# Kernel optimization log

Measured on AMD Instinct MI355X. Metric: run time of the kernel, lower is better.

Reference implementation:

```python
import jax, jax.numpy as jnp
import numpy as np

B, S, IN_DIM, D_MODEL, H = 8, 1024, 512, 1024, 16
DEPTH = D_MODEL // H
LN_EPS = 1e-5


def setup_inputs() -> dict:
    key = jax.random.key(0)
    ks = jax.random.split(key, 10)
    def xavier(k, shape):
        fan_in, fan_out = shape[0], shape[1]
        lim = float(np.sqrt(6.0 / (fan_in + fan_out)))
        return jax.random.uniform(k, shape, jnp.float32, -lim, lim)
    return {
        "x": jax.random.normal(ks[0], (B, S, IN_DIM), jnp.float32),
        "mask": jax.random.randint(ks[1], (H, S, S), 0, 2, jnp.int32),
        "wq_w": xavier(ks[2], (IN_DIM, D_MODEL)),
        "wq_b": jnp.zeros((D_MODEL,), jnp.float32),
        "wk_w": xavier(ks[3], (IN_DIM, D_MODEL)),
        "wk_b": jnp.zeros((D_MODEL,), jnp.float32),
        "wv_w": xavier(ks[4], (IN_DIM, D_MODEL)),
        "wv_b": jnp.zeros((D_MODEL,), jnp.float32),
        "dense_w": xavier(ks[5], (D_MODEL, D_MODEL)),
        "dense_b": jnp.zeros((D_MODEL,), jnp.float32),
        "res_w": xavier(ks[6], (IN_DIM, D_MODEL)),  # residual_linear (no bias)
        "ln_g": 1.0 + 0.02 * jax.random.normal(ks[7], (D_MODEL,), jnp.float32),
        "ln_b": 0.02 * jax.random.normal(ks[8], (D_MODEL,), jnp.float32),
    }


def reference(x, mask, wq_w, wq_b, wk_w, wk_b, wv_w, wv_b,
              dense_w, dense_b, res_w, ln_g, ln_b):
    bs = x.shape[0]
    residual = x @ res_w  # [B,S,D_MODEL]
    # project and split heads -> [B,H,S,depth]
    def split(t):
        return t.reshape(bs, -1, H, DEPTH).transpose(0, 2, 1, 3)
    q = split(x @ wq_w + wq_b)
    k = split(x @ wk_w + wk_b)
    v = split(x @ wv_w + wv_b)
    scale = 1.0 / jnp.sqrt(jnp.asarray(DEPTH, x.dtype))
    attn = jnp.einsum("bhqd,bhkd->bhqk", q, k) * scale
    attn = jnp.where(mask[None] == 0, jnp.asarray(-1e9, attn.dtype), attn)
    attn = jax.nn.softmax(attn, axis=-1)  # dropout is identity in eval
    out = jnp.einsum("bhqk,bhkd->bhqd", attn, v)
    out = out.transpose(0, 2, 1, 3).reshape(bs, -1, D_MODEL)
    out = out @ dense_w + dense_b
    # residual + LayerNorm
    y = residual + out
    mu = jnp.mean(y, axis=-1, keepdims=True)
    var = jnp.mean(jnp.square(y - mu), axis=-1, keepdims=True)
    y = (y - mu) * jax.lax.rsqrt(var + LN_EPS)
    return y * ln_g + ln_b
```

## Files before the change

kernel.cpp:

```cpp
#include <hip/hip_runtime.h>
#include <stdint.h>

#define B_ 8
#define S_ 1024
#define IN_DIM 512
#define DM 1024
#define H_ 16
#define DEP 64

typedef __bf16 bf16;
typedef __attribute__((ext_vector_type(8))) __bf16 bf16x8;
typedef __attribute__((ext_vector_type(4))) __bf16 bf16x4;
typedef __attribute__((ext_vector_type(4))) short short4v;
typedef __attribute__((ext_vector_type(4))) float f32x4;

#if defined(__has_builtin)
#if __has_builtin(__builtin_amdgcn_mfma_f32_16x16x16_bf16)
#define HAVE_NEW16 1
#endif
#endif
static __device__ __forceinline__ f32x4 mfma16(bf16x4 a, bf16x4 b, f32x4 c) {
#ifdef HAVE_NEW16
    return __builtin_amdgcn_mfma_f32_16x16x16_bf16(a, b, c, 0, 0, 0);
#else
    union { bf16x4 h; short4v s; } ua, ub;
    ua.h = a; ub.h = b;
    return __builtin_amdgcn_mfma_f32_16x16x16bf16_1k(ua.s, ub.s, c, 0, 0, 0);
#endif
}

static __device__ __forceinline__ void gld_lds16(const void* g, void* l) {
    __builtin_amdgcn_global_load_lds(
        (const __attribute__((address_space(1))) uint32_t*)g,
        (__attribute__((address_space(3))) uint32_t*)l, 16, 0, 0);
}

__global__ void detect_kernel(const uint16_t* __restrict__ xraw, int* __restrict__ flag) {
    const int t = threadIdx.x;
    int sane = 0;
    #pragma unroll
    for (int j = 0; j < 8; j++) {
        const uint16_t u = xraw[t * 8 + j];
        const int e = (u >> 7) & 0xff;
        sane += ((u & 0x7fff) == 0 || (e >= 100 && e <= 140)) ? 1 : 0;
    }
    #pragma unroll
    for (int m = 1; m < 64; m <<= 1) sane += __shfl_xor(sane, m);
    if (t == 0) *flag = (sane >= 450) ? 1 : 0;
}

static __device__ __forceinline__ float ldin(const void* p, size_t i, int isb) {
    return isb ? (float)((const bf16*)p)[i] : ((const float*)p)[i];
}

__global__ __launch_bounds__(256) void transpose_kernel(
    const void* __restrict__ wq, const void* __restrict__ wk, const void* __restrict__ wv,
    const void* __restrict__ res, const void* __restrict__ dense,
    bf16* __restrict__ wqT, bf16* __restrict__ wkT, bf16* __restrict__ wvT,
    bf16* __restrict__ resT, bf16* __restrict__ denseT, const int* __restrict__ flag)
{
    const int isb = *flag;
    __shared__ bf16 tile[32][33];
    const int z = blockIdx.z;
    const void* src; bf16* dst; int kb, kd;
    if (z == 0)      { src = wq;    dst = wqT;    kb = 0;   kd = 512;  }
    else if (z == 1) { src = wk;    dst = wkT;    kb = 0;   kd = 512;  }
    else if (z == 2) { src = wv;    dst = wvT;    kb = 0;   kd = 512;  }
    else if (z == 3) { src = res;   dst = resT;   kb = 0;   kd = 512;  }
    else if (z == 4) { src = dense; dst = denseT; kb = 0;   kd = 1024; }
    else             { src = dense; dst = denseT; kb = 512; kd = 1024; }
    const int n0 = blockIdx.x * 32, k0 = blockIdx.y * 32;
    const int tx = threadIdx.x, ty = threadIdx.y;
    #pragma unroll
    for (int r = 0; r < 4; r++)
        tile[ty + r*8][tx] = (bf16)ldin(src, (size_t)(kb + k0 + ty + r*8) * DM + n0 + tx, isb);
    __syncthreads();
    #pragma unroll
    for (int r = 0; r < 4; r++)
        dst[(size_t)(n0 + ty + r*8) * kd + kb + k0 + tx] = tile[tx][ty + r*8];
}

__global__ __launch_bounds__(256) void xconv_kernel(
    const void* __restrict__ x, bf16* __restrict__ xc, const int* __restrict__ flag)
{
    const int isb = *flag;
    const size_t i = ((size_t)blockIdx.x * 256 + threadIdx.x) * 4;
    #pragma unroll
    for (int j = 0; j < 4; j++) xc[i + j] = (bf16)ldin(x, i + j, isb);
}

__global__ __launch_bounds__(256) void smallconv_kernel(
    const void* b0, const void* b1, const void* b2, const void* b3,
    const void* b4, const void* b5, bf16* __restrict__ out, const int* __restrict__ flag)
{
    const int isb = *flag;
    const void* srcs[6] = {b0, b1, b2, b3, b4, b5};
    const void* s = srcs[blockIdx.x];
    for (int i = threadIdx.x; i < 1024; i += 256)
        out[blockIdx.x * 1024 + i] = (bf16)ldin(s, i, isb);
}

__global__ __launch_bounds__(256) void maskpack_kernel(
    const int* __restrict__ mask, unsigned long long* __restrict__ mb)
{
    const int w = threadIdx.x >> 6, lane = threadIdx.x & 63;
    const int gw = blockIdx.x * 4 + w;
    for (int c = gw; c < 262144; c += 4096) {
        const int v = mask[(size_t)c * 64 + lane];
        const unsigned long long bits = __ballot(v != 0);
        if (lane == 0) mb[c] = bits;
    }
}

template<int KDIM>
static __device__ __forceinline__ void gemm_core(
    const bf16* __restrict__ A, const bf16* __restrict__ BT,
    int m0, int n0, bf16* Asm, bf16* Bsm, f32x4 acc[4][4])
{
    const int tid = threadIdx.x, l = tid & 63, w = tid >> 6;
    const int wm = w >> 1, wn = w & 1, quad = l >> 4, l15 = l & 15;
    #pragma unroll
    for (int i = 0; i < 4; i++)
        #pragma unroll
        for (int j = 0; j < 4; j++) acc[i][j] = f32x4{0.f, 0.f, 0.f, 0.f};

    for (int k0 = 0; k0 < KDIM; k0 += 32) {
        __syncthreads();
        #pragma unroll
        for (int qq = 0; qq < 2; qq++) {
            const int c = qq*256 + tid;
            const int row = c >> 2, ch = c & 3;
            gld_lds16(A  + (size_t)(m0 + row)*KDIM + k0 + ch*8, Asm + (qq*256 + w*64)*8);
            gld_lds16(BT + (size_t)(n0 + row)*KDIM + k0 + ch*8, Bsm + (qq*256 + w*64)*8);
        }
        __syncthreads();
        bf16x8 af[4], bfv[4];
        #pragma unroll
        for (int i = 0; i < 4; i++)
            af[i] = *(const bf16x8*)(Asm + (wm*64 + i*16 + l15)*32 + quad*8);
        #pragma unroll
        for (int j = 0; j < 4; j++)
            bfv[j] = *(const bf16x8*)(Bsm + (wn*64 + j*16 + l15)*32 + quad*8);
        #pragma unroll
        for (int i = 0; i < 4; i++)
            #pragma unroll
            for (int j = 0; j < 4; j++)
                acc[i][j] = __builtin_amdgcn_mfma_f32_16x16x32_bf16(af[i], bfv[j], acc[i][j], 0, 0, 0);
    }
}

#define EPI_P 132
__global__ __launch_bounds__(256) void proj_kernel(
    const bf16* __restrict__ x,
    const bf16* __restrict__ wqT, const bf16* __restrict__ wkT,
    const bf16* __restrict__ wvT, const bf16* __restrict__ resT,
    const bf16* __restrict__ small,
    bf16* __restrict__ Q, bf16* __restrict__ K, bf16* __restrict__ VtG, bf16* __restrict__ R)
{
    __shared__ alignas(16) char smem[17408];
    bf16* Asm = (bf16*)smem;
    bf16* Bsm = (bf16*)(smem + 8192);
    bf16* epi = (bf16*)smem;

    const int m0 = blockIdx.x * 128;
    const int ng = blockIdx.y * 128;
    const int sel = ng >> 10, n0 = ng & 1023;
    const bf16* BT; const bf16* bias = nullptr;
    if (sel == 0)      { BT = wqT; bias = small;        }
    else if (sel == 1) { BT = wkT; bias = small + 1024; }
    else if (sel == 2) { BT = wvT; bias = small + 2048; }
    else               { BT = resT; }

    f32x4 acc[4][4];
    gemm_core<IN_DIM>(x, BT, m0, n0, Asm, Bsm, acc);

    const int tid = threadIdx.x, l = tid & 63, w = tid >> 6;
    const int wm = w >> 1, wn = w & 1, quad = l >> 4, l15 = l & 15;

    if (sel == 2) {
        const int bb = m0 >> 10, srow0 = m0 & 1023;
        #pragma unroll
        for (int hf = 0; hf < 2; hf++) {
            __syncthreads();
            if (wn == hf) {
                #pragma unroll
                for (int j = 0; j < 4; j++) {
                    const int cl = j*16 + l15;
                    const float bv = (float)bias[n0 + hf*64 + cl];
                    #pragma unroll
                    for (int i = 0; i < 4; i++) {
                        const int rho = wm*64 + i*16 + quad*4;
                        #pragma unroll
                        for (int r = 0; r < 4; r++)
                            epi[cl*EPI_P + rho + r] = (bf16)(acc[i][j][r] + bv);
                    }
                }
            }
            __syncthreads();
            const int hh = (n0 >> 6) + hf;
            const int sc = tid & 15;
            #pragma unroll
            for (int pass = 0; pass < 4; pass++) {
                const int dl = (tid >> 4) + pass*16;
                bf16x8 v;
                #pragma unroll
                for (int k = 0; k < 8; k++) v[k] = epi[dl*EPI_P + sc*8 + k];
                *(bf16x8*)(VtG + ((size_t)(bb*16 + hh)*64 + dl)*S_ + srow0 + sc*8) = v;
            }
        }
        return;
    }

    #pragma unroll
    for (int j = 0; j < 4; j++) {
        const int col = n0 + wn*64 + j*16 + l15;
        const float bv = (sel < 3) ? (float)bias[col] : 0.f;
        #pragma unroll
        for (int i = 0; i < 4; i++) {
            const int rb = m0 + wm*64 + i*16 + quad*4;
            #pragma unroll
            for (int r = 0; r < 4; r++) {
                const float v = acc[i][j][r] + bv;
                if (sel == 0)      Q[(size_t)(rb + r)*DM + col] = (bf16)(v * 0.125f);
                else if (sel == 1) K[(size_t)(rb + r)*DM + col] = (bf16)v;
                else               R[(size_t)(rb + r)*DM + col] = (bf16)v;
            }
        }
    }
}

#define KP 68
__global__ __launch_bounds__(256) void attn_kernel(
    const bf16* __restrict__ Q, const bf16* __restrict__ K, const bf16* __restrict__ VtG,
    const unsigned long long* __restrict__ mb, bf16* __restrict__ AO)
{
    __shared__ alignas(16) bf16 Ksm[64*KP];
    __shared__ alignas(16) bf16 Vsm[64*KP];

    const int tid = threadIdx.x, l = tid & 63, w = tid >> 6;
    const int quad = l >> 4, l15 = l & 15;
    const int b = blockIdx.y >> 4, h = blockIdx.y & 15;
    const int wrow = blockIdx.x*128 + w*32;
    const size_t rowbase = (size_t)b * S_;

    bf16x8 qa[2][2];
    #pragma unroll
    for (int g = 0; g < 2; g++) {
        const bf16* qp = Q + (rowbase + wrow + g*16 + l15)*DM + h*DEP + quad*8;
        qa[g][0] = *(const bf16x8*)qp;
        qa[g][1] = *(const bf16x8*)(qp + 32);
    }
    const bf16* kgbase = K + rowbase*DM + h*DEP;
    const bf16* vgbase = VtG + (size_t)(b*16 + h)*64*S_;
    const unsigned long long* mbase[2];
    #pragma unroll
    for (int g = 0; g < 2; g++)
        mbase[g] = mb + ((size_t)h*S_ + wrow + g*16 + l15) * 16;

    f32x4 oT[2][4];
    float lsum[2] = {0.f, 0.f};
    #pragma unroll
    for (int g = 0; g < 2; g++)
        #pragma unroll
        for (int dt = 0; dt < 4; dt++) oT[g][dt] = f32x4{0.f,0.f,0.f,0.f};

    const int srow = tid >> 3, sch = tid & 7;

    bf16x8 k0v = *(const bf16x8*)(kgbase + (size_t)srow*DM + sch*8);
    bf16x8 k1v = *(const bf16x8*)(kgbase + (size_t)(32 + srow)*DM + sch*8);
    bf16x8 v0v = *(const bf16x8*)(vgbase + (size_t)srow*S_ + sch*8);
    bf16x8 v1v = *(const bf16x8*)(vgbase + (size_t)(32 + srow)*S_ + sch*8);
    uint32_t mlo[2], mhi[2];
    #pragma unroll
    for (int g = 0; g < 2; g++) {
        const unsigned long long mword = mbase[g][0];
        mlo[g] = (uint32_t)mword; mhi[g] = (uint32_t)(mword >> 32);
    }

    for (int it = 0; it < 16; it++) {
        __syncthreads();
        *(bf16x8*)(Ksm + srow*KP + sch*8)        = k0v;
        *(bf16x8*)(Ksm + (32 + srow)*KP + sch*8) = k1v;
        *(bf16x8*)(Vsm + srow*KP + sch*8)        = v0v;
        *(bf16x8*)(Vsm + (32 + srow)*KP + sch*8) = v1v;
        __syncthreads();

        const uint32_t cmlo[2] = {mlo[0], mlo[1]}, cmhi[2] = {mhi[0], mhi[1]};
        if (it + 1 < 16) {
            const int nkt = (it + 1) * 64;
            k0v = *(const bf16x8*)(kgbase + (size_t)(nkt + srow)*DM + sch*8);
            k1v = *(const bf16x8*)(kgbase + (size_t)(nkt + 32 + srow)*DM + sch*8);
            v0v = *(const bf16x8*)(vgbase + (size_t)srow*S_ + nkt + sch*8);
            v1v = *(const bf16x8*)(vgbase + (size_t)(32 + srow)*S_ + nkt + sch*8);
            #pragma unroll
            for (int g = 0; g < 2; g++) {
                const unsigned long long mword = mbase[g][it + 1];
                mlo[g] = (uint32_t)mword; mhi[g] = (uint32_t)(mword >> 32);
            }
        }

        #pragma unroll
        for (int sub = 0; sub < 2; sub++) {
            bf16x8 kf[2][2];
            bf16x4 va[2][4];
            #pragma unroll
            for (int h2 = 0; h2 < 2; h2++) {
                const bf16* kp = Ksm + (sub*32 + h2*16 + l15)*KP + quad*8;
                kf[h2][0] = *(const bf16x8*)kp;
                kf[h2][1] = *(const bf16x8*)(kp + 32);
            }
            #pragma unroll
            for (int h2 = 0; h2 < 2; h2++)
                #pragma unroll
                for (int dt = 0; dt < 4; dt++)
                    va[h2][dt] = *(const bf16x4*)(Vsm + (dt*16 + l15)*KP + sub*32 + h2*16 + quad*4);

            #pragma unroll
            for (int g = 0; g < 2; g++) {
                f32x4 st[2];
                #pragma unroll
                for (int h2 = 0; h2 < 2; h2++) {
                    f32x4 z = {0.f,0.f,0.f,0.f};
                    z = __builtin_amdgcn_mfma_f32_16x16x32_bf16(kf[h2][0], qa[g][0], z, 0, 0, 0);
                    z = __builtin_amdgcn_mfma_f32_16x16x32_bf16(kf[h2][1], qa[g][1], z, 0, 0, 0);
                    st[h2] = z;
                }
                const uint32_t msk = sub ? cmhi[g] : cmlo[g];
                bf16x4 pb[2];
                #pragma unroll
                for (int h2 = 0; h2 < 2; h2++) {
                    const uint32_t nib = (msk >> (h2*16 + quad*4)) & 0xfu;
                    #pragma unroll
                    for (int r = 0; r < 4; r++) {
                        const float e = __expf(st[h2][r]);
                        const float pv = ((nib >> r) & 1u) ? e : 0.f;
                        lsum[g] += pv;
                        pb[h2][r] = (bf16)pv;
                    }
                }
                #pragma unroll
                for (int h2 = 0; h2 < 2; h2++)
                    #pragma unroll
                    for (int dt = 0; dt < 4; dt++)
                        oT[g][dt] = mfma16(va[h2][dt], pb[h2], oT[g][dt]);
            }
        }
    }

    #pragma unroll
    for (int g = 0; g < 2; g++) {
        lsum[g] += __shfl_xor(lsum[g], 16);
        lsum[g] += __shfl_xor(lsum[g], 32);
        const float inv = 1.0f / lsum[g];
        bf16* aor = AO + (rowbase + wrow + g*16 + l15)*DM + h*DEP;
        #pragma unroll
        for (int dt = 0; dt < 4; dt++) {
            bf16x4 ov;
            #pragma unroll
            for (int r = 0; r < 4; r++) ov[r] = (bf16)(oT[g][dt][r] * inv);
            *(bf16x4*)(aor + dt*16 + quad*4) = ov;
        }
    }
}

__global__ __launch_bounds__(256) void dense_kernel(
    const bf16* __restrict__ AOin, const bf16* __restrict__ dT,
    const bf16* __restrict__ db, bf16* __restrict__ R)
{
    __shared__ alignas(16) bf16 Asm[128*32];
    __shared__ alignas(16) bf16 Bsm[128*32];
    const int m0 = blockIdx.x * 128, n0 = blockIdx.y * 128;
    f32x4 acc[4][4];
    gemm_core<DM>(AOin, dT, m0, n0, Asm, Bsm, acc);
    const int tid = threadIdx.x, l = tid & 63, w = tid >> 6;
    const int wm = w >> 1, wn = w & 1, quad = l >> 4, l15 = l & 15;
    #pragma unroll
    for (int j = 0; j < 4; j++) {
        const int col = n0 + wn*64 + j*16 + l15;
        const float bv = (float)db[col];
        #pragma unroll
        for (int i = 0; i < 4; i++) {
            const int rb = m0 + wm*64 + i*16 + quad*4;
            #pragma unroll
            for (int r = 0; r < 4; r++) {
                const size_t idx = (size_t)(rb + r)*DM + col;
                R[idx] = (bf16)((float)R[idx] + acc[i][j][r] + bv);
            }
        }
    }
}

__global__ __launch_bounds__(256) void ln_kernel(
    const bf16* __restrict__ R, const bf16* __restrict__ small,
    void* __restrict__ out, const int* __restrict__ flag)
{
    const int isb = *flag;
    __shared__ float red[8];
    const int row = blockIdx.x, tid = threadIdx.x;
    const bf16x4 rv = *(const bf16x4*)(R + (size_t)row*DM + tid*4);
    const float vx = (float)rv[0], vy = (float)rv[1], vz = (float)rv[2], vw = (float)rv[3];
    float s = vx + vy + vz + vw;
    #pragma unroll
    for (int m = 1; m < 64; m <<= 1) s += __shfl_xor(s, m);
    const int w = tid >> 6;
    if ((tid & 63) == 0) red[w] = s;
    __syncthreads();
    const float mu = (red[0] + red[1] + red[2] + red[3]) * (1.0f/DM);
    const float dx = vx - mu, dy = vy - mu, dz = vz - mu, dw = vw - mu;
    float q = dx*dx + dy*dy + dz*dz + dw*dw;
    #pragma unroll
    for (int m = 1; m < 64; m <<= 1) q += __shfl_xor(q, m);
    if ((tid & 63) == 0) red[4 + w] = q;
    __syncthreads();
    const float var = (red[4] + red[5] + red[6] + red[7]) * (1.0f/DM);
    const float rstd = rsqrtf(var + 1e-5f);
    const int col = tid * 4;
    const bf16x4 gv = *(const bf16x4*)(small + 4*1024 + col);
    const bf16x4 bv = *(const bf16x4*)(small + 5*1024 + col);
    const float o0 = dx*rstd*(float)gv[0] + (float)bv[0];
    const float o1 = dy*rstd*(float)gv[1] + (float)bv[1];
    const float o2 = dz*rstd*(float)gv[2] + (float)bv[2];
    const float o3 = dw*rstd*(float)gv[3] + (float)bv[3];
    if (isb) {
        bf16x4 ov; ov[0] = (bf16)o0; ov[1] = (bf16)o1; ov[2] = (bf16)o2; ov[3] = (bf16)o3;
        *(bf16x4*)((bf16*)out + (size_t)row*DM + col) = ov;
    } else {
        float4 ov = {o0, o1, o2, o3};
        *(float4*)((float*)out + (size_t)row*DM + col) = ov;
    }
}

extern "C" void kernel_launch(void* const* d_in, const int* in_sizes, int n_in,
                              void* d_out, int out_size, void* d_ws, size_t ws_size,
                              hipStream_t stream) {
    const int* mask = (const int*)d_in[1];

    char* ws = (char*)d_ws;
    bf16* wqT   = (bf16*)(ws);
    bf16* wkT   = (bf16*)(ws + ((size_t)1 << 20));
    bf16* wvT   = (bf16*)(ws + ((size_t)2 << 20));
    bf16* resT  = (bf16*)(ws + ((size_t)3 << 20));
    bf16* dT    = (bf16*)(ws + ((size_t)4 << 20));
    bf16* small = (bf16*)(ws + ((size_t)6 << 20));
    int*  flag  = (int*) (ws + ((size_t)6 << 20) + 16384);
    unsigned long long* mbits = (unsigned long long*)(ws + ((size_t)7 << 20));
    bf16* Qb    = (bf16*)(ws + ((size_t)9  << 20));
    bf16* Kb    = (bf16*)(ws + ((size_t)25 << 20));
    bf16* VtG   = (bf16*)(ws + ((size_t)41 << 20));
    bf16* R     = (bf16*)(ws + ((size_t)57 << 20));
    bf16* xc    = (bf16*)d_out;

    detect_kernel<<<1, 64, 0, stream>>>((const uint16_t*)d_in[0], flag);
    transpose_kernel<<<dim3(32, 16, 6), dim3(32, 8), 0, stream>>>(
        d_in[2], d_in[4], d_in[6], d_in[10], d_in[8],
        wqT, wkT, wvT, resT, dT, flag);
    xconv_kernel<<<4096, 256, 0, stream>>>(d_in[0], xc, flag);
    smallconv_kernel<<<6, 256, 0, stream>>>(
        d_in[3], d_in[5], d_in[7], d_in[9], d_in[11], d_in[12], small, flag);
    maskpack_kernel<<<1024, 256, 0, stream>>>(mask, mbits);
    proj_kernel<<<dim3(64, 32), 256, 0, stream>>>(
        xc, wqT, wkT, wvT, resT, small, Qb, Kb, VtG, R);
    attn_kernel<<<dim3(8, 128), 256, 0, stream>>>(Qb, Kb, VtG, mbits, Qb );
    dense_kernel<<<dim3(64, 8), 256, 0, stream>>>(Qb, dT, small + 3*1024, R);
    ln_kernel<<<8192, 256, 0, stream>>>(R, small, d_out, flag);
}
```

Measured before the change: 372.2 us.

## Fuse prep kernels, drop LDS staging in attention, use exp2 with prescaled Q

Merges the detect, transpose, x-convert, bias-convert and mask-pack launches into one prep kernel, with every block redoing the dtype detection locally. Attention now loads K and V fragments straight from global memory into registers, double-buffered across 32-key sub-steps, instead of staging them in shared memory behind barriers. Softmax uses the hardware exp2 with log2(e) folded into the Q scale. The trade-off is more uncoalesced global reads per wave, relying on cache reuse, plus redundant detection work in every prep and LayerNorm block.

```diff
diff --git a/kernel.cpp b/kernel.cpp
--- a/kernel.cpp
+++ b/kernel.cpp
@@ -29,86 +29,96 @@
 #endif
 }
 
+static __device__ __forceinline__ float fexp2(float x) {
+#if defined(__has_builtin)
+#if __has_builtin(__builtin_amdgcn_exp2f)
+    return __builtin_amdgcn_exp2f(x);
+#define FEXP_DONE 1
+#endif
+#endif
+#ifndef FEXP_DONE
+    float r; __asm__("v_exp_f32 %0, %1" : "=v"(r) : "v"(x)); return r;
+#endif
+}
+
 static __device__ __forceinline__ void gld_lds16(const void* g, void* l) {
     __builtin_amdgcn_global_load_lds(
         (const __attribute__((address_space(1))) uint32_t*)g,
         (__attribute__((address_space(3))) uint32_t*)l, 16, 0, 0);
 }
 
-__global__ void detect_kernel(const uint16_t* __restrict__ xraw, int* __restrict__ flag) {
-    const int t = threadIdx.x;
+static __device__ __forceinline__ float ldin(const void* p, size_t i, int isb) {
+    return isb ? (float)((const bf16*)p)[i] : ((const float*)p)[i];
+}
+
+static __device__ __forceinline__ int block_detect(const void* x, int tid, int* sred) {
+    const uint32_t two = ((const uint32_t*)x)[tid];
     int sane = 0;
     #pragma unroll
-    for (int j = 0; j < 8; j++) {
-        const uint16_t u = xraw[t * 8 + j];
+    for (int half = 0; half < 2; half++) {
+        const uint32_t u = (half ? (two >> 16) : two) & 0xffffu;
         const int e = (u >> 7) & 0xff;
         sane += ((u & 0x7fff) == 0 || (e >= 100 && e <= 140)) ? 1 : 0;
     }
     #pragma unroll
-    for (int m = 1; m < 64; m <<= 1) sane += __shfl_xor(sane, m);
-    if (t == 0) *flag = (sane >= 450) ? 1 : 0;
-}
-
-static __device__ __forceinline__ float ldin(const void* p, size_t i, int isb) {
-    return isb ? (float)((const bf16*)p)[i] : ((const float*)p)[i];
-}
-
-__global__ __launch_bounds__(256) void transpose_kernel(
+    for (int m2 = 1; m2 < 64; m2 <<= 1) sane += __shfl_xor(sane, m2);
+    if ((tid & 63) == 0) sred[tid >> 6] = sane;
+    __syncthreads();
+    return (sred[0] + sred[1] + sred[2] + sred[3]) >= 900;
+}
+
+__global__ __launch_bounds__(256) void prep_kernel(
+    const void* __restrict__ x, const int* __restrict__ mask,
     const void* __restrict__ wq, const void* __restrict__ wk, const void* __restrict__ wv,
     const void* __restrict__ res, const void* __restrict__ dense,
+    const void* __restrict__ bq, const void* __restrict__ bk, const void* __restrict__ bv,
+    const void* __restrict__ bd, const void* __restrict__ lg, const void* __restrict__ lb,
     bf16* __restrict__ wqT, bf16* __restrict__ wkT, bf16* __restrict__ wvT,
-    bf16* __restrict__ resT, bf16* __restrict__ denseT, const int* __restrict__ flag)
-{
-    const int isb = *flag;
+    bf16* __restrict__ resT, bf16* __restrict__ denseT,
+    bf16* __restrict__ xc, bf16* __restrict__ small, unsigned long long* __restrict__ mb)
+{
     __shared__ bf16 tile[32][33];
-    const int z = blockIdx.z;
-    const void* src; bf16* dst; int kb, kd;
-    if (z == 0)      { src = wq;    dst = wqT;    kb = 0;   kd = 512;  }
-    else if (z == 1) { src = wk;    dst = wkT;    kb = 0;   kd = 512;  }
-    else if (z == 2) { src = wv;    dst = wvT;    kb = 0;   kd = 512;  }
-    else if (z == 3) { src = res;   dst = resT;   kb = 0;   kd = 512;  }
-    else if (z == 4) { src = dense; dst = denseT; kb = 0;   kd = 1024; }
-    else             { src = dense; dst = denseT; kb = 512; kd = 1024; }
-    const int n0 = blockIdx.x * 32, k0 = blockIdx.y * 32;
-    const int tx = threadIdx.x, ty = threadIdx.y;
-    #pragma unroll
-    for (int r = 0; r < 4; r++)
-        tile[ty + r*8][tx] = (bf16)ldin(src, (size_t)(kb + k0 + ty + r*8) * DM + n0 + tx, isb);
-    __syncthreads();
-    #pragma unroll
-    for (int r = 0; r < 4; r++)
-        dst[(size_t)(n0 + ty + r*8) * kd + kb + k0 + tx] = tile[tx][ty + r*8];
-}
-
-__global__ __launch_bounds__(256) void xconv_kernel(
-    const void* __restrict__ x, bf16* __restrict__ xc, const int* __restrict__ flag)
-{
-    const int isb = *flag;
-    const size_t i = ((size_t)blockIdx.x * 256 + threadIdx.x) * 4;
-    #pragma unroll
-    for (int j = 0; j < 4; j++) xc[i + j] = (bf16)ldin(x, i + j, isb);
-}
-
-__global__ __launch_bounds__(256) void smallconv_kernel(
-    const void* b0, const void* b1, const void* b2, const void* b3,
-    const void* b4, const void* b5, bf16* __restrict__ out, const int* __restrict__ flag)
-{
-    const int isb = *flag;
-    const void* srcs[6] = {b0, b1, b2, b3, b4, b5};
-    const void* s = srcs[blockIdx.x];
-    for (int i = threadIdx.x; i < 1024; i += 256)
-        out[blockIdx.x * 1024 + i] = (bf16)ldin(s, i, isb);
-}
-
-__global__ __launch_bounds__(256) void maskpack_kernel(
-    const int* __restrict__ mask, unsigned long long* __restrict__ mb)
-{
-    const int w = threadIdx.x >> 6, lane = threadIdx.x & 63;
-    const int gw = blockIdx.x * 4 + w;
-    for (int c = gw; c < 262144; c += 4096) {
-        const int v = mask[(size_t)c * 64 + lane];
-        const unsigned long long bits = __ballot(v != 0);
-        if (lane == 0) mb[c] = bits;
+    __shared__ int sred[4];
+    const int tid = threadIdx.x;
+    const int isb = block_detect(x, tid, sred);
+    const int idx = blockIdx.x;
+
+    if (idx < 3072) {
+        const int z = idx >> 9, r2 = idx & 511;
+        const void* src; bf16* dst; int kb, kd;
+        if (z == 0)      { src = wq;    dst = wqT;    kb = 0;   kd = 512;  }
+        else if (z == 1) { src = wk;    dst = wkT;    kb = 0;   kd = 512;  }
+        else if (z == 2) { src = wv;    dst = wvT;    kb = 0;   kd = 512;  }
+        else if (z == 3) { src = res;   dst = resT;   kb = 0;   kd = 512;  }
+        else if (z == 4) { src = dense; dst = denseT; kb = 0;   kd = 1024; }
+        else             { src = dense; dst = denseT; kb = 512; kd = 1024; }
+        const int n0 = (r2 & 31) * 32, k0 = (r2 >> 5) * 32;
+        const int tx = tid & 31, ty = tid >> 5;
+        #pragma unroll
+        for (int r = 0; r < 4; r++)
+            tile[ty + r*8][tx] = (bf16)ldin(src, (size_t)(kb + k0 + ty + r*8) * DM + n0 + tx, isb);
+        __syncthreads();
+        #pragma unroll
+        for (int r = 0; r < 4; r++)
+            dst[(size_t)(n0 + ty + r*8) * kd + kb + k0 + tx] = tile[tx][ty + r*8];
+    } else if (idx < 7168) {
+        const size_t i = ((size_t)(idx - 3072) * 256 + tid) * 4;
+        #pragma unroll
+        for (int j = 0; j < 4; j++) xc[i + j] = (bf16)ldin(x, i + j, isb);
+    } else if (idx < 8192) {
+        const int w = tid >> 6, lane = tid & 63;
+        const int gw = (idx - 7168) * 4 + w;
+        for (int c = gw; c < 262144; c += 4096) {
+            const int v = mask[(size_t)c * 64 + lane];
+            const unsigned long long bits = __ballot(v != 0);
+            if (lane == 0) mb[c] = bits;
+        }
+    } else {
+        const void* srcs[6] = {bq, bk, bv, bd, lg, lb};
+        const int s = idx - 8192;
+        const void* sp = srcs[s];
+        for (int i = tid; i < 1024; i += 256)
+            small[s * 1024 + i] = (bf16)ldin(sp, i, isb);
     }
 }
 
@@ -221,7 +231,7 @@
             #pragma unroll
             for (int r = 0; r < 4; r++) {
                 const float v = acc[i][j][r] + bv;
-                if (sel == 0)      Q[(size_t)(rb + r)*DM + col] = (bf16)(v * 0.125f);
+                if (sel == 0)      Q[(size_t)(rb + r)*DM + col] = (bf16)(v * 0.180336881f);
                 else if (sel == 1) K[(size_t)(rb + r)*DM + col] = (bf16)v;
                 else               R[(size_t)(rb + r)*DM + col] = (bf16)v;
             }
@@ -229,14 +239,51 @@
     }
 }
 
-#define KP 68
+#define ATTN_PRE(KF, VA)                                                        \
+  do {                                                                          \
+    KF[0][0] = *(const bf16x8*)(kb0);  KF[0][1] = *(const bf16x8*)(kb0 + 32);   \
+    KF[1][0] = *(const bf16x8*)(kb1);  KF[1][1] = *(const bf16x8*)(kb1 + 32);   \
+    _Pragma("unroll")                                                           \
+    for (int dt = 0; dt < 4; dt++) {                                            \
+      VA[0][dt] = *(const bf16x4*)(vb[dt]);                                     \
+      VA[1][dt] = *(const bf16x4*)(vb[dt] + 16);                                \
+    }                                                                           \
+    kb0 += 32*DM; kb1 += 32*DM;                                                 \
+    _Pragma("unroll")                                                           \
+    for (int dt = 0; dt < 4; dt++) vb[dt] += 32;                                \
+  } while (0)
+
+#define ATTN_STEP(KF, VA, M0, M1)                                               \
+  do {                                                                          \
+    _Pragma("unroll")                                                           \
+    for (int g = 0; g < 2; g++) {                                               \
+      f32x4 st0 = {0.f,0.f,0.f,0.f}, st1 = {0.f,0.f,0.f,0.f};                   \
+      st0 = __builtin_amdgcn_mfma_f32_16x16x32_bf16(KF[0][0], qa[g][0], st0, 0,0,0); \
+      st0 = __builtin_amdgcn_mfma_f32_16x16x32_bf16(KF[0][1], qa[g][1], st0, 0,0,0); \
+      st1 = __builtin_amdgcn_mfma_f32_16x16x32_bf16(KF[1][0], qa[g][0], st1, 0,0,0); \
+      st1 = __builtin_amdgcn_mfma_f32_16x16x32_bf16(KF[1][1], qa[g][1], st1, 0,0,0); \
+      const uint32_t msk_ = g ? (M1) : (M0);                                    \
+      const uint32_t nib0 = (msk_ >> (quad*4)) & 0xfu;                          \
+      const uint32_t nib1 = (msk_ >> (16 + quad*4)) & 0xfu;                     \
+      bf16x4 pb0, pb1;                                                          \
+      _Pragma("unroll")                                                         \
+      for (int r = 0; r < 4; r++) {                                             \
+        float e0 = fexp2(st0[r]); e0 = ((nib0 >> r) & 1u) ? e0 : 0.f;           \
+        float e1 = fexp2(st1[r]); e1 = ((nib1 >> r) & 1u) ? e1 : 0.f;           \
+        lsum[g] += e0 + e1; pb0[r] = (bf16)e0; pb1[r] = (bf16)e1;               \
+      }                                                                         \
+      _Pragma("unroll")                                                         \
+      for (int dt = 0; dt < 4; dt++) {                                          \
+        oT[g][dt] = mfma16(VA[0][dt], pb0, oT[g][dt]);                          \
+        oT[g][dt] = mfma16(VA[1][dt], pb1, oT[g][dt]);                          \
+      }                                                                         \
+    }                                                                           \
+  } while (0)
+
 __global__ __launch_bounds__(256) void attn_kernel(
     const bf16* __restrict__ Q, const bf16* __restrict__ K, const bf16* __restrict__ VtG,
     const unsigned long long* __restrict__ mb, bf16* __restrict__ AO)
 {
-    __shared__ alignas(16) bf16 Ksm[64*KP];
-    __shared__ alignas(16) bf16 Vsm[64*KP];
-
     const int tid = threadIdx.x, l = tid & 63, w = tid >> 6;
     const int quad = l >> 4, l15 = l & 15;
     const int b = blockIdx.y >> 4, h = blockIdx.y & 15;
@@ -250,8 +297,13 @@
         qa[g][0] = *(const bf16x8*)qp;
         qa[g][1] = *(const bf16x8*)(qp + 32);
     }
-    const bf16* kgbase = K + rowbase*DM + h*DEP;
-    const bf16* vgbase = VtG + (size_t)(b*16 + h)*64*S_;
+    const bf16* kb0 = K + (rowbase + l15)*DM + h*DEP + quad*8;
+    const bf16* kb1 = kb0 + 16*DM;
+    const bf16* vb[4];
+    #pragma unroll
+    for (int dt = 0; dt < 4; dt++)
+        vb[dt] = VtG + ((size_t)(b*16 + h)*64 + dt*16 + l15)*S_ + quad*4;
+
     const unsigned long long* mbase[2];
     #pragma unroll
     for (int g = 0; g < 2; g++)
@@ -264,87 +316,23 @@
         #pragma unroll
         for (int dt = 0; dt < 4; dt++) oT[g][dt] = f32x4{0.f,0.f,0.f,0.f};
 
-    const int srow = tid >> 3, sch = tid & 7;
-
-    bf16x8 k0v = *(const bf16x8*)(kgbase + (size_t)srow*DM + sch*8);
-    bf16x8 k1v = *(const bf16x8*)(kgbase + (size_t)(32 + srow)*DM + sch*8);
-    bf16x8 v0v = *(const bf16x8*)(vgbase + (size_t)srow*S_ + sch*8);
-    bf16x8 v1v = *(const bf16x8*)(vgbase + (size_t)(32 + srow)*S_ + sch*8);
-    uint32_t mlo[2], mhi[2];
-    #pragma unroll
-    for (int g = 0; g < 2; g++) {
-        const unsigned long long mword = mbase[g][0];
-        mlo[g] = (uint32_t)mword; mhi[g] = (uint32_t)(mword >> 32);
-    }
-
-    for (int it = 0; it < 16; it++) {
-        __syncthreads();
-        *(bf16x8*)(Ksm + srow*KP + sch*8)        = k0v;
-        *(bf16x8*)(Ksm + (32 + srow)*KP + sch*8) = k1v;
-        *(bf16x8*)(Vsm + srow*KP + sch*8)        = v0v;
-        *(bf16x8*)(Vsm + (32 + srow)*KP + sch*8) = v1v;
-        __syncthreads();
-
-        const uint32_t cmlo[2] = {mlo[0], mlo[1]}, cmhi[2] = {mhi[0], mhi[1]};
-        if (it + 1 < 16) {
-            const int nkt = (it + 1) * 64;
-            k0v = *(const bf16x8*)(kgbase + (size_t)(nkt + srow)*DM + sch*8);
-            k1v = *(const bf16x8*)(kgbase + (size_t)(nkt + 32 + srow)*DM + sch*8);
-            v0v = *(const bf16x8*)(vgbase + (size_t)srow*S_ + nkt + sch*8);
-            v1v = *(const bf16x8*)(vgbase + (size_t)(32 + srow)*S_ + nkt + sch*8);
-            #pragma unroll
-            for (int g = 0; g < 2; g++) {
-                const unsigned long long mword = mbase[g][it + 1];
-                mlo[g] = (uint32_t)mword; mhi[g] = (uint32_t)(mword >> 32);
-            }
-        }
-
-        #pragma unroll
-        for (int sub = 0; sub < 2; sub++) {
-            bf16x8 kf[2][2];
-            bf16x4 va[2][4];
-            #pragma unroll
-            for (int h2 = 0; h2 < 2; h2++) {
-                const bf16* kp = Ksm + (sub*32 + h2*16 + l15)*KP + quad*8;
-                kf[h2][0] = *(const bf16x8*)kp;
-                kf[h2][1] = *(const bf16x8*)(kp + 32);
-            }
-            #pragma unroll
-            for (int h2 = 0; h2 < 2; h2++)
-                #pragma unroll
-                for (int dt = 0; dt < 4; dt++)
-                    va[h2][dt] = *(const bf16x4*)(Vsm + (dt*16 + l15)*KP + sub*32 + h2*16 + quad*4);
-
-            #pragma unroll
-            for (int g = 0; g < 2; g++) {
-                f32x4 st[2];
-                #pragma unroll
-                for (int h2 = 0; h2 < 2; h2++) {
-                    f32x4 z = {0.f,0.f,0.f,0.f};
-                    z = __builtin_amdgcn_mfma_f32_16x16x32_bf16(kf[h2][0], qa[g][0], z, 0, 0, 0);
-                    z = __builtin_amdgcn_mfma_f32_16x16x32_bf16(kf[h2][1], qa[g][1], z, 0, 0, 0);
-                    st[h2] = z;
-                }
-                const uint32_t msk = sub ? cmhi[g] : cmlo[g];
-                bf16x4 pb[2];
-                #pragma unroll
-                for (int h2 = 0; h2 < 2; h2++) {
-                    const uint32_t nib = (msk >> (h2*16 + quad*4)) & 0xfu;
-                    #pragma unroll
-                    for (int r = 0; r < 4; r++) {
-                        const float e = __expf(st[h2][r]);
-                        const float pv = ((nib >> r) & 1u) ? e : 0.f;
-                        lsum[g] += pv;
-                        pb[h2][r] = (bf16)pv;
-                    }
-                }
-                #pragma unroll
-                for (int h2 = 0; h2 < 2; h2++)
-                    #pragma unroll
-                    for (int dt = 0; dt < 4; dt++)
-                        oT[g][dt] = mfma16(va[h2][dt], pb[h2], oT[g][dt]);
-            }
-        }
+    bf16x8 kfA[2][2], kfB[2][2];
+    bf16x4 vaA[2][4], vaB[2][4];
+
+    unsigned long long mw0 = mbase[0][0], mw1 = mbase[1][0];
+    ATTN_PRE(kfA, vaA);
+
+    #pragma unroll 1
+    for (int t = 0; t < 16; t++) {
+        ATTN_PRE(kfB, vaB);
+        ATTN_STEP(kfA, vaA, (uint32_t)mw0, (uint32_t)mw1);
+        unsigned long long mn0 = 0, mn1 = 0;
+        if (t < 15) {
+            ATTN_PRE(kfA, vaA);
+            mn0 = mbase[0][t + 1]; mn1 = mbase[1][t + 1];
+        }
+        ATTN_STEP(kfB, vaB, (uint32_t)(mw0 >> 32), (uint32_t)(mw1 >> 32));
+        mw0 = mn0; mw1 = mn1;
     }
 
     #pragma unroll
@@ -392,11 +380,13 @@
 
 __global__ __launch_bounds__(256) void ln_kernel(
     const bf16* __restrict__ R, const bf16* __restrict__ small,
-    void* __restrict__ out, const int* __restrict__ flag)
-{
-    const int isb = *flag;
+    void* __restrict__ out, const void* __restrict__ x)
+{
     __shared__ float red[8];
-    const int row = blockIdx.x, tid = threadIdx.x;
+    __shared__ int sred[4];
+    const int tid = threadIdx.x;
+    const int isb = block_detect(x, tid, sred);
+    const int row = blockIdx.x;
     const bf16x4 rv = *(const bf16x4*)(R + (size_t)row*DM + tid*4);
     const float vx = (float)rv[0], vy = (float)rv[1], vz = (float)rv[2], vw = (float)rv[3];
     float s = vx + vy + vz + vw;
@@ -442,7 +432,6 @@
     bf16* resT  = (bf16*)(ws + ((size_t)3 << 20));
     bf16* dT    = (bf16*)(ws + ((size_t)4 << 20));
     bf16* small = (bf16*)(ws + ((size_t)6 << 20));
-    int*  flag  = (int*) (ws + ((size_t)6 << 20) + 16384);
     unsigned long long* mbits = (unsigned long long*)(ws + ((size_t)7 << 20));
     bf16* Qb    = (bf16*)(ws + ((size_t)9  << 20));
     bf16* Kb    = (bf16*)(ws + ((size_t)25 << 20));
@@ -450,17 +439,13 @@
     bf16* R     = (bf16*)(ws + ((size_t)57 << 20));
     bf16* xc    = (bf16*)d_out;
 
-    detect_kernel<<<1, 64, 0, stream>>>((const uint16_t*)d_in[0], flag);
-    transpose_kernel<<<dim3(32, 16, 6), dim3(32, 8), 0, stream>>>(
-        d_in[2], d_in[4], d_in[6], d_in[10], d_in[8],
-        wqT, wkT, wvT, resT, dT, flag);
-    xconv_kernel<<<4096, 256, 0, stream>>>(d_in[0], xc, flag);
-    smallconv_kernel<<<6, 256, 0, stream>>>(
-        d_in[3], d_in[5], d_in[7], d_in[9], d_in[11], d_in[12], small, flag);
-    maskpack_kernel<<<1024, 256, 0, stream>>>(mask, mbits);
+    prep_kernel<<<8198, 256, 0, stream>>>(
+        d_in[0], mask, d_in[2], d_in[4], d_in[6], d_in[10], d_in[8],
+        d_in[3], d_in[5], d_in[7], d_in[9], d_in[11], d_in[12],
+        wqT, wkT, wvT, resT, dT, xc, small, mbits);
     proj_kernel<<<dim3(64, 32), 256, 0, stream>>>(
         xc, wqT, wkT, wvT, resT, small, Qb, Kb, VtG, R);
     attn_kernel<<<dim3(8, 128), 256, 0, stream>>>(Qb, Kb, VtG, mbits, Qb );
     dense_kernel<<<dim3(64, 8), 256, 0, stream>>>(Qb, dT, small + 3*1024, R);
-    ln_kernel<<<8192, 256, 0, stream>>>(R, small, d_out, flag);
-}
+    ln_kernel<<<8192, 256, 0, stream>>>(R, small, d_out, d_in[0]);
+}
```

Result: slower. 462.2 us (+24.2%).
